# Kernel optimization log

Hardware: AMD Instinct MI355X
Metric: run time of the kernel (lower is better)

## Reference

```python
import jax, jax.numpy as jnp
import numpy as np

B = 65536
D = 512            # resnet18 fc.in_features
NUM_CLASSES = 512  # size of batch_centers
LEVELS = [2048, 1024, 512]


def setup_inputs() -> dict:
    key = jax.random.key(0)
    ks = jax.random.split(key, 8)
    x = jax.random.normal(ks[0], (B, D), dtype=jnp.float32)
    labels = jax.random.randint(ks[1], (B,), 0, NUM_CLASSES, dtype=jnp.int64)
    W0 = jax.random.normal(ks[2], (LEVELS[0], D), dtype=jnp.float32) * 0.02
    b0 = jnp.zeros((LEVELS[0],), dtype=jnp.float32)
    W1 = jax.random.normal(ks[3], (LEVELS[1], LEVELS[0]), dtype=jnp.float32) * 0.02
    b1 = jnp.zeros((LEVELS[1],), dtype=jnp.float32)
    W2 = jax.random.normal(ks[4], (LEVELS[2], LEVELS[1]), dtype=jnp.float32) * 0.02
    b2 = jnp.zeros((LEVELS[2],), dtype=jnp.float32)
    lambda_values = jnp.array([1e-3, 1.0, 1.0, 1.0], dtype=jnp.float32)
    return {"x": x, "W0": W0, "b0": b0, "W1": W1, "b1": b1,
            "W2": W2, "b2": b2, "lambda_values": lambda_values,
            "labels": labels}


def _cross_entropy(logits, labels):
    # mean over batch of -log p(label) (torch CrossEntropyLoss default)
    logp = jax.nn.log_softmax(logits, axis=-1)
    nll = -jnp.take_along_axis(logp, labels[:, None], axis=-1)[:, 0]
    return jnp.mean(nll)


def reference(x, W0, b0, W1, b1, W2, b2, lambda_values, labels):
    # --- per-class scatter-mean centers (vectorized segment reduce) ---
    sums = jax.ops.segment_sum(x, labels, num_segments=NUM_CLASSES)
    counts = jax.ops.segment_sum(jnp.ones((x.shape[0],), x.dtype), labels,
                                 num_segments=NUM_CLASSES)
    centers = jnp.where(counts[:, None] > 0,
                        sums / jnp.maximum(counts, 1.0)[:, None],
                        0.0)  # classes absent from batch keep zero centers
    # --- gather-diff center loss: sum_i ||x_i - c_{y_i}||^2 ---
    diff = x - centers[labels]
    center_loss = jnp.sum(diff * diff)
    # --- cascaded classification heads, CE at each level ---
    h = x
    losses = []
    for W, b in ((W0, b0), (W1, b1), (W2, b2)):
        h = h @ W.T + b
        losses.append(_cross_entropy(h, labels))
    classification_losses = jnp.stack(losses)
    return lambda_values[0] * center_loss + jnp.dot(lambda_values[1:],
                                                    classification_losses)
```

## Files before the change

### kernel.cpp

```cpp
#include <hip/hip_runtime.h>
#include <cstdint>
#include <cstddef>

using f32x4  = __attribute__((ext_vector_type(4))) float;
using i32x4v = __attribute__((ext_vector_type(4))) int;
using i32x8v = __attribute__((ext_vector_type(8))) int;

__device__ __forceinline__ unsigned char f2fp8(float f) {
  return (unsigned char)(__builtin_amdgcn_cvt_pk_fp8_f32(f, f, 0, false) & 0xff);
}

__device__ __forceinline__ float fp8b0(unsigned int w) {
  return __builtin_amdgcn_cvt_f32_fp8(w, 0);
}
__device__ __forceinline__ float fp8b1(unsigned int w) {
  return __builtin_amdgcn_cvt_f32_fp8(w, 1);
}
__device__ __forceinline__ float fp8b2(unsigned int w) {
  return __builtin_amdgcn_cvt_f32_fp8(w, 2);
}
__device__ __forceinline__ float fp8b3(unsigned int w) {
  return __builtin_amdgcn_cvt_f32_fp8(w, 3);
}

__device__ __forceinline__ float waveRed(float v) {
#pragma unroll
  for (int m = 32; m >= 1; m >>= 1) v += __shfl_xor(v, m, 64);
  return v;
}

__device__ __forceinline__ void gload16(const void* g, void* l) {
  __builtin_amdgcn_global_load_lds(
      (__attribute__((address_space(1))) uint32_t*)(uintptr_t)g,
      (__attribute__((address_space(3))) uint32_t*)(uint32_t*)l,
      16, 0, 0);
}

__global__ __launch_bounds__(256) void prep_w(
    const float4* __restrict__ W1, const float4* __restrict__ W2,
    const float4* __restrict__ W0f4, const float* __restrict__ W0,
    const float* __restrict__ b0,
    uint32_t* __restrict__ W1_8, uint32_t* __restrict__ W2_8,
    uint32_t* __restrict__ W0_8, unsigned char* __restrict__ W0t8,
    float* __restrict__ zr, int zwords, float* __restrict__ biascat) {
  __shared__ unsigned char t8[64][65];
  const int b = blockIdx.x;
  const int tid = threadIdx.x;
  if (b < 1024) {
    for (int i = b * 256 + tid; i < 524288; i += 1024 * 256) {
      float4 v = W1[i];
      int p = __builtin_amdgcn_cvt_pk_fp8_f32(v.x, v.y, 0, false);
      p = __builtin_amdgcn_cvt_pk_fp8_f32(v.z, v.w, p, true);
      W1_8[i] = (uint32_t)p;
    }
  } else if (b < 1280) {
    for (int i = (b - 1024) * 256 + tid; i < 131072; i += 256 * 256) {
      float4 v = W2[i];
      int p = __builtin_amdgcn_cvt_pk_fp8_f32(v.x, v.y, 0, false);
      p = __builtin_amdgcn_cvt_pk_fp8_f32(v.z, v.w, p, true);
      W2_8[i] = (uint32_t)p;
    }
  } else if (b < 1536) {
    for (int i = (b - 1280) * 256 + tid; i < 262144; i += 256 * 256) {
      float4 v = W0f4[i];
      int p = __builtin_amdgcn_cvt_pk_fp8_f32(v.x, v.y, 0, false);
      p = __builtin_amdgcn_cvt_pk_fp8_f32(v.z, v.w, p, true);
      W0_8[i] = (uint32_t)p;
    }
  } else if (b < 1792) {
    const int t = b - 1536;
    const int r0 = (t >> 3) * 64, c0 = (t & 7) * 64;
#pragma unroll
    for (int p = 0; p < 16; ++p) {
      const int row = p * 4 + (tid >> 6), col = tid & 63;
      t8[row][col] = f2fp8(W0[(size_t)(r0 + row) * 512 + c0 + col]);
    }
    __syncthreads();
#pragma unroll
    for (int p = 0; p < 16; ++p) {
      const int oc = p * 4 + (tid >> 6), orr = tid & 63;
      W0t8[(size_t)(c0 + oc) * 2048 + r0 + orr] = t8[orr][oc];
    }
  } else {
    const int zb = (zwords + 255) >> 8;
    if (b < 1792 + zb) {
      const int i = (b - 1792) * 256 + tid;
      if (i < zwords) zr[i] = 0.f;
    } else {
      const int i = (b - 1792 - zb) * 256 + tid;
      if (i < 2048) biascat[i] = b0[i];
    }
  }
}

__global__ __launch_bounds__(256) void count_k(const int* __restrict__ lab,
                                               int* __restrict__ counts, int n) {
  __shared__ int h[512];
  for (int i = threadIdx.x; i < 512; i += 256) h[i] = 0;
  __syncthreads();
  for (int i = blockIdx.x * 256 + threadIdx.x; i < n; i += gridDim.x * 256)
    atomicAdd(&h[lab[i]], 1);
  __syncthreads();
  for (int i = threadIdx.x; i < 512; i += 256) {
    int v = h[i];
    if (v) atomicAdd(&counts[i], v);
  }
}

__global__ void prefix_k(const int* __restrict__ counts, int* __restrict__ offsets,
                         int* __restrict__ cursor, int nc) {
  const int lane = threadIdx.x;
  int base = 0;
  for (int c0 = 0; c0 < nc; c0 += 64) {
    int v = counts[c0 + lane];
    int x = v;
#pragma unroll
    for (int d = 1; d < 64; d <<= 1) {
      int y = __shfl_up(x, d, 64);
      if (lane >= d) x += y;
    }
    int excl = base + x - v;
    offsets[c0 + lane] = excl;
    cursor[c0 + lane] = excl;
    base += __shfl(x, 63, 64);
  }
}

__global__ void scatter_k(const int* __restrict__ lab, int* __restrict__ cursor,
                          int* __restrict__ buckets, int n) {
  for (int i = blockIdx.x * 256 + threadIdx.x; i < n; i += gridDim.x * 256) {
    int pos = atomicAdd(&cursor[lab[i]], 1);
    buckets[pos] = i;
  }
}

__global__ __launch_bounds__(256) void csum_k(const float* __restrict__ x,
    const int* __restrict__ buckets, const int* __restrict__ offsets,
    const int* __restrict__ counts, float* __restrict__ centers,
    float* __restrict__ scal) {
  const int c = blockIdx.x >> 2, q = blockIdx.x & 3;
  const int cnt = counts[c];
  const int t = threadIdx.x;
  float sx = 0.f, sy = 0.f, ssq = 0.f;
  int lo = 0, hi = 0;
  if (cnt) {
    const int beg = offsets[c];
    lo = beg + (cnt * q) / 4;
    hi = beg + (cnt * (q + 1)) / 4;
    for (int i = lo; i < hi; ++i) {
      const int row = buckets[i];
      const float2 v = ((const float2*)(x + (size_t)row * 512))[t];
      sx += v.x;
      sy += v.y;
      ssq += v.x * v.x + v.y * v.y;
    }
    if (lo < hi) {
      atomicAdd(&centers[c * 512 + 2 * t], sx);
      atomicAdd(&centers[c * 512 + 2 * t + 1], sy);
    }
  }
  ssq = waveRed(ssq);
  __shared__ float red[4];
  if ((t & 63) == 0) red[t >> 6] = ssq;
  __syncthreads();
  if (t == 0) {
    const float s = red[0] + red[1] + red[2] + red[3];
    if (s != 0.f) atomicAdd(&scal[0], s);
  }
}

__global__ __launch_bounds__(256) void cnorm_k(const float* __restrict__ centers,
    const int* __restrict__ counts, float* __restrict__ out) {
  const int c = blockIdx.x;
  const int cnt = counts[c];
  if (cnt == 0) return;
  const float2 v = ((const float2*)(centers + (size_t)c * 512))[threadIdx.x];
  float ssq = v.x * v.x + v.y * v.y;
  ssq = waveRed(ssq);
  __shared__ float red[4];
  if ((threadIdx.x & 63) == 0) red[threadIdx.x >> 6] = ssq;
  __syncthreads();
  if (threadIdx.x == 0)
    atomicAdd(out, (red[0] + red[1] + red[2] + red[3]) / (float)cnt);
}

__global__ __launch_bounds__(256) void matvec_k(const float* __restrict__ W,
    const float* __restrict__ vin, const float* __restrict__ badd,
    float* __restrict__ vout, int K) {
  int row = blockIdx.x;
  float s = 0.f;
  for (int k = threadIdx.x; k < K; k += 256) s += W[(size_t)row * K + k] * vin[k];
  s = waveRed(s);
  __shared__ float red[4];
  if ((threadIdx.x & 63) == 0) red[threadIdx.x >> 6] = s;
  __syncthreads();
  if (threadIdx.x == 0) vout[row] = red[0] + red[1] + red[2] + red[3] + badd[row];
}

__global__ void pk_k(const float* __restrict__ centers,
                     const unsigned char* __restrict__ Bcat8,
                     const float* __restrict__ biascat,
                     const int* __restrict__ counts, float* __restrict__ scal) {
  const int b = blockIdx.x;
  const int lvl = b >> 9;
  const int c = b & 511;
  const int lane = threadIdx.x;
  const int cbase = (lvl == 0) ? 0 : (lvl == 1) ? 2048 : 3072;
  const float4* S = (const float4*)(centers + (size_t)c * 512);
  const uint2 wb = ((const uint2*)(Bcat8 + (size_t)(cbase + c) * 512))[lane];
  const float4 s0 = S[lane * 2];
  const float4 s1 = S[lane * 2 + 1];
  float s = s0.x * fp8b0(wb.x) + s0.y * fp8b1(wb.x) +
            s0.z * fp8b2(wb.x) + s0.w * fp8b3(wb.x) +
            s1.x * fp8b0(wb.y) + s1.y * fp8b1(wb.y) +
            s1.z * fp8b2(wb.y) + s1.w * fp8b3(wb.y);
  s = waveRed(s);
  if (lane == 0)
    atomicAdd(&scal[5 + lvl], s + (float)counts[c] * biascat[cbase + c]);
}

__global__ __launch_bounds__(256) void gemm8_w(
    const unsigned char* __restrict__ A8, const unsigned char* __restrict__ B8,
    int M, int N, int K, unsigned char* __restrict__ C8,
    unsigned char* __restrict__ Ct8) {
  __shared__ __align__(16) unsigned char As[128 * 128];
  __shared__ __align__(16) unsigned char Bs[128 * 128];
  const int tid = threadIdx.x;
  const int lane = tid & 63;
  const int wave = tid >> 6;
  const int lane16 = lane & 15;
  const int quad = lane >> 4;
  const int wm = (wave >> 1) * 64;
  const int wn = (wave & 1) * 64;
  const int m0 = blockIdx.y * 128;
  const int n0 = blockIdx.x * 128;

  f32x4 acc[4][4] = {};

  int srow[4], goff[4];
#pragma unroll
  for (int q = 0; q < 4; ++q) {
    const int s = tid + q * 256;
    const int row = s >> 3;
    const int c16 = s & 7;
    srow[q] = row;
    goff[q] = (((c16 >> 1) ^ (row & 3)) << 5) + ((c16 & 1) << 4);
  }

  for (int kt = 0; kt < K; kt += 128) {
#pragma unroll
    for (int q = 0; q < 4; ++q) {
      const int s = tid + q * 256;
      gload16(A8 + (size_t)(m0 + srow[q]) * K + kt + goff[q], &As[s * 16]);
      gload16(B8 + (size_t)(n0 + srow[q]) * K + kt + goff[q], &Bs[s * 16]);
    }
    __syncthreads();
    i32x8v a8[4], b8[4];
#pragma unroll
    for (int i = 0; i < 4; ++i) {
      const int row = i * 16 + lane16;
      const int sc = quad ^ (row & 3);
      const unsigned char* pa = &As[row * 128 + sc * 32];
      const i32x4v lo = *(const i32x4v*)pa;
      const i32x4v hi = *(const i32x4v*)(pa + 16);
      a8[i] = (i32x8v){lo[0], lo[1], lo[2], lo[3], hi[0], hi[1], hi[2], hi[3]};
    }
#pragma unroll
    for (int j = 0; j < 4; ++j) {
      const int row = j * 16 + lane16;
      const int sc = quad ^ (row & 3);
      const unsigned char* pb = &Bs[row * 128 + sc * 32];
      const i32x4v lo = *(const i32x4v*)pb;
      const i32x4v hi = *(const i32x4v*)(pb + 16);
      b8[j] = (i32x8v){lo[0], lo[1], lo[2], lo[3], hi[0], hi[1], hi[2], hi[3]};
    }
#pragma unroll
    for (int i = 0; i < 4; ++i)
#pragma unroll
      for (int j = 0; j < 4; ++j)
        acc[i][j] = __builtin_amdgcn_mfma_scale_f32_16x16x128_f8f6f4(
            a8[i], b8[j], acc[i][j], 0, 0, 0, 0x7f7f7f7f, 0, 0x7f7f7f7f);
    __syncthreads();
  }
#pragma unroll
  for (int i = 0; i < 4; ++i)
#pragma unroll
    for (int r = 0; r < 4; ++r) {
      const int rowg = m0 + wm + i * 16 + quad * 4 + r;
#pragma unroll
      for (int j = 0; j < 4; ++j) {
        const int colg = n0 + wn + j * 16 + lane16;
        const unsigned char v8 = f2fp8(acc[i][j][r]);
        C8[(size_t)rowg * N + colg] = v8;
        if (Ct8) Ct8[(size_t)colg * M + rowg] = v8;
      }
    }
}

__global__ void reorder_k(const unsigned char* __restrict__ in,
                          unsigned char* __restrict__ out) {
  const int id = blockIdx.x * 256 + threadIdx.x;
  const int col = id >> 4;
  const int k32 = id & 15;
  const int kt = k32 >> 2, quad = k32 & 3;
  const size_t src = (size_t)col * 512 + k32 * 32;
  const size_t dst = (size_t)(col >> 6) * 32768 + (size_t)kt * 8192 +
                     (size_t)((col >> 4) & 3) * 2048 +
                     (size_t)(quad * 16 + (col & 15)) * 32;
  const uint4 a = *(const uint4*)(in + src);
  const uint4 b = *(const uint4*)(in + src + 16);
  *(uint4*)(out + dst) = a;
  *(uint4*)(out + dst + 16) = b;
}

__global__ __launch_bounds__(256, 2) void gemm_ce8(
    const float* __restrict__ x, const unsigned char* __restrict__ Bp,
    const float* __restrict__ bias, float* __restrict__ scal) {
  const int tid = threadIdx.x;
  const int lane = tid & 63;
  const int wave = tid >> 6;
  const int lane16 = lane & 15;
  const int quad = lane >> 4;
  const int m0 = blockIdx.x * 128 + wave * 32;

  i32x8v a[2][4];
#pragma unroll
  for (int i = 0; i < 2; ++i) {
    const float* xr = x + (size_t)(m0 + i * 16 + lane16) * 512 + quad * 32;
#pragma unroll
    for (int kt = 0; kt < 4; ++kt) {
      const float4* p4 = (const float4*)(xr + kt * 128);
      int d[8];
#pragma unroll
      for (int p = 0; p < 8; ++p) {
        const float4 f = p4[p];
        int w_ = __builtin_amdgcn_cvt_pk_fp8_f32(f.x, f.y, 0, false);
        w_ = __builtin_amdgcn_cvt_pk_fp8_f32(f.z, f.w, w_, true);
        d[p] = w_;
      }
      a[i][kt] = (i32x8v){d[0], d[1], d[2], d[3], d[4], d[5], d[6], d[7]};
    }
  }

  const unsigned char* bp = Bp + lane * 32;
  i32x8v bc[4], bn[4];
#pragma unroll
  for (int j = 0; j < 4; ++j) bc[j] = *(const i32x8v*)(bp + j * 2048);
  bp += 8192;

  float es[8];
#pragma unroll
  for (int k = 0; k < 8; ++k) es[k] = 0.f;

  int tile = 0;
#pragma unroll 1
  for (int lvl = 0; lvl < 3; ++lvl) {
    const int nt = (lvl == 0) ? 32 : (lvl == 1) ? 16 : 8;
#pragma unroll 1
    for (int t = 0; t < nt; ++t, ++tile) {
      f32x4 acc[2][4] = {};
#pragma unroll
      for (int kt2 = 0; kt2 < 2; ++kt2) {
#pragma unroll
        for (int j = 0; j < 4; ++j) bn[j] = *(const i32x8v*)(bp + j * 2048);
        bp += 8192;
#pragma unroll
        for (int i = 0; i < 2; ++i)
#pragma unroll
          for (int j = 0; j < 4; ++j)
            acc[i][j] = __builtin_amdgcn_mfma_scale_f32_16x16x128_f8f6f4(
                a[i][kt2 * 2], bc[j], acc[i][j], 0, 0, 0, 0x7f7f7f7f, 0,
                0x7f7f7f7f);
#pragma unroll
        for (int j = 0; j < 4; ++j) bc[j] = *(const i32x8v*)(bp + j * 2048);
        bp += 8192;
#pragma unroll
        for (int i = 0; i < 2; ++i)
#pragma unroll
          for (int j = 0; j < 4; ++j)
            acc[i][j] = __builtin_amdgcn_mfma_scale_f32_16x16x128_f8f6f4(
                a[i][kt2 * 2 + 1], bn[j], acc[i][j], 0, 0, 0, 0x7f7f7f7f, 0,
                0x7f7f7f7f);
      }
      float bj[4];
#pragma unroll
      for (int j = 0; j < 4; ++j) bj[j] = bias[tile * 64 + j * 16 + lane16];
#pragma unroll
      for (int i = 0; i < 2; ++i)
#pragma unroll
        for (int r = 0; r < 4; ++r) {
          float e = 0.f;
#pragma unroll
          for (int j = 0; j < 4; ++j) e += __expf(acc[i][j][r] + bj[j]);
          es[i * 4 + r] += e;
        }
      __builtin_amdgcn_s_barrier();
    }
    float ls = 0.f;
#pragma unroll
    for (int k = 0; k < 8; ++k) {
      float tot = es[k];
      tot += __shfl_xor(tot, 1, 64);
      tot += __shfl_xor(tot, 2, 64);
      tot += __shfl_xor(tot, 4, 64);
      tot += __shfl_xor(tot, 8, 64);
      if (lane16 == 0) ls += __logf(tot);
      es[k] = 0.f;
    }
    ls = waveRed(ls);
    if (lane == 0) atomicAdd(&scal[2 + lvl], ls);
  }
}

__global__ void fin_k(const float* __restrict__ scal, const float* __restrict__ lam,
                      float* __restrict__ out, float invB) {
  if (threadIdx.x == 0 && blockIdx.x == 0)
    out[0] = lam[0] * (scal[0] - scal[1]) +
             (lam[1] * (scal[2] - scal[5]) + lam[2] * (scal[3] - scal[6]) +
              lam[3] * (scal[4] - scal[7])) * invB;
}

extern "C" void kernel_launch(void* const* d_in, const int* in_sizes, int n_in,
                              void* d_out, int out_size, void* d_ws, size_t ws_size,
                              hipStream_t stream) {
  const float* x   = (const float*)d_in[0];
  const float* W0  = (const float*)d_in[1];
  const float* b0  = (const float*)d_in[2];
  const float* W1  = (const float*)d_in[3];
  const float* b1  = (const float*)d_in[4];
  const float* W2  = (const float*)d_in[5];
  const float* b2  = (const float*)d_in[6];
  const float* lam = (const float*)d_in[7];
  const int*   lab = (const int*)d_in[8];

  const int Bsz = in_sizes[8];
  const int D   = in_sizes[0] / Bsz;
  const int N0  = in_sizes[2];
  const int N1  = in_sizes[4];
  const int N2  = in_sizes[6];
  const int Ncat = N0 + N1 + N2;
  const int NCLS = 512;

  char* w = (char*)d_ws;
  size_t off = 0;
  auto alloc = [&](size_t bytes) -> void* {
    void* p = w + off;
    off += (bytes + 255) & ~(size_t)255;
    return p;
  };

  unsigned char* Bcat8 = (unsigned char*)alloc((size_t)Ncat * D);
  unsigned char* Bp    = (unsigned char*)alloc((size_t)Ncat * D + 16384);
  unsigned char* W1_8  = (unsigned char*)alloc((size_t)N1 * N0);
  unsigned char* W2_8  = (unsigned char*)alloc((size_t)N2 * N1);
  unsigned char* W0t8  = (unsigned char*)alloc((size_t)D * N0);
  unsigned char* M1t8  = (unsigned char*)alloc((size_t)D * N1);
  float* biascat = (float*)alloc((size_t)Ncat * 4);
  int* offsets = (int*)alloc(NCLS * 4);
  int* cursor  = (int*)alloc(NCLS * 4);
  int* buckets = (int*)alloc((size_t)Bsz * 4);
  const int zwords = NCLS + 8 + NCLS * 512;
  char* zr = (char*)alloc((size_t)zwords * 4);
  int*   counts  = (int*)zr;
  float* scal    = (float*)(zr + NCLS * 4);
  float* centers = (float*)(zr + NCLS * 4 + 32);
  (void)ws_size; (void)n_in; (void)out_size;

  const int zb = (zwords + 255) / 256;
  prep_w<<<dim3(1792 + zb + 8), dim3(256), 0, stream>>>(
      (const float4*)W1, (const float4*)W2, (const float4*)W0, W0, b0,
      (uint32_t*)W1_8, (uint32_t*)W2_8, (uint32_t*)Bcat8, W0t8,
      (float*)zr, zwords, biascat);

  count_k<<<dim3(32), dim3(256), 0, stream>>>(lab, counts, Bsz);
  prefix_k<<<dim3(1), dim3(64), 0, stream>>>(counts, offsets, cursor, NCLS);
  scatter_k<<<dim3(256), dim3(256), 0, stream>>>(lab, cursor, buckets, Bsz);
  csum_k<<<dim3(4 * NCLS), dim3(256), 0, stream>>>(x, buckets, offsets, counts,
                                                   centers, scal);
  cnorm_k<<<dim3(NCLS), dim3(256), 0, stream>>>(centers, counts, &scal[1]);

  matvec_k<<<dim3(N1), dim3(256), 0, stream>>>(W1, b0, b1, biascat + N0, N0);
  matvec_k<<<dim3(N2), dim3(256), 0, stream>>>(W2, biascat + N0, b2, biascat + N0 + N1, N1);

  gemm8_w<<<dim3(D / 128, N1 / 128), dim3(256), 0, stream>>>(
      W1_8, W0t8, N1, D, N0, Bcat8 + (size_t)N0 * D, M1t8);
  gemm8_w<<<dim3(D / 128, N2 / 128), dim3(256), 0, stream>>>(
      W2_8, M1t8, N2, D, N1, Bcat8 + (size_t)(N0 + N1) * D, nullptr);

  reorder_k<<<dim3(Ncat * D / 32 / 256), dim3(256), 0, stream>>>(Bcat8, Bp);

  pk_k<<<dim3(3 * NCLS), dim3(64), 0, stream>>>(centers, Bcat8, biascat,
                                                counts, scal);

  gemm_ce8<<<dim3(Bsz / 128), dim3(256), 0, stream>>>(x, Bp, biascat, scal);

  fin_k<<<dim3(1), dim3(64), 0, stream>>>(scal, lam, (float*)d_out, 1.f / (float)Bsz);
}
```

Baseline: 539.7 us.

## Stage B fragments through LDS with async prefetch; replace center atomics with partials

The fused GEMM+CE kernel now streams the packed fp8 weight fragments into a four-slot shared-memory ring using async global-to-LDS loads, waiting with vmcnt and barriers, instead of each wave loading its B fragments directly from global into registers. The bias vector is cached in shared memory once per block. The reorder kernel changes the packed layout to split each lane's 32 bytes into two 16-byte halves to match the 16-byte async loads. Separately, the per-class center sums write four partial buffers that cnorm_k reduces, replacing float atomics. The ring adds LDS traffic and a barrier per k-step, and may lower occupancy.

```diff
diff --git a/kernel.cpp b/kernel.cpp
--- a/kernel.cpp
+++ b/kernel.cpp
@@ -136,17 +136,15 @@
 
 __global__ __launch_bounds__(256) void csum_k(const float* __restrict__ x,
     const int* __restrict__ buckets, const int* __restrict__ offsets,
-    const int* __restrict__ counts, float* __restrict__ centers,
+    const int* __restrict__ counts, float* __restrict__ centers4,
     float* __restrict__ scal) {
   const int c = blockIdx.x >> 2, q = blockIdx.x & 3;
   const int cnt = counts[c];
   const int t = threadIdx.x;
   float sx = 0.f, sy = 0.f, ssq = 0.f;
-  int lo = 0, hi = 0;
   if (cnt) {
     const int beg = offsets[c];
-    lo = beg + (cnt * q) / 4;
-    hi = beg + (cnt * (q + 1)) / 4;
+    const int lo = beg + (cnt * q) / 4, hi = beg + (cnt * (q + 1)) / 4;
     for (int i = lo; i < hi; ++i) {
       const int row = buckets[i];
       const float2 v = ((const float2*)(x + (size_t)row * 512))[t];
@@ -154,11 +152,9 @@
       sy += v.y;
       ssq += v.x * v.x + v.y * v.y;
     }
-    if (lo < hi) {
-      atomicAdd(&centers[c * 512 + 2 * t], sx);
-      atomicAdd(&centers[c * 512 + 2 * t + 1], sy);
-    }
-  }
+  }
+  float2* dst = (float2*)(centers4 + (size_t)((c << 2) + q) * 512);
+  dst[t] = make_float2(sx, sy);
   ssq = waveRed(ssq);
   __shared__ float red[4];
   if ((t & 63) == 0) red[t >> 6] = ssq;
@@ -169,18 +165,25 @@
   }
 }
 
-__global__ __launch_bounds__(256) void cnorm_k(const float* __restrict__ centers,
-    const int* __restrict__ counts, float* __restrict__ out) {
+__global__ __launch_bounds__(256) void cnorm_k(const float* __restrict__ centers4,
+    float* __restrict__ centers, const int* __restrict__ counts,
+    float* __restrict__ out) {
   const int c = blockIdx.x;
+  const int t = threadIdx.x;
+  const float2* p = (const float2*)(centers4 + (size_t)(c << 2) * 512);
+  float2 s = p[t];
+  float2 s1 = p[t + 256], s2 = p[t + 512], s3 = p[t + 768];
+  s.x += s1.x + s2.x + s3.x;
+  s.y += s1.y + s2.y + s3.y;
+  ((float2*)(centers + (size_t)c * 512))[t] = s;
   const int cnt = counts[c];
   if (cnt == 0) return;
-  const float2 v = ((const float2*)(centers + (size_t)c * 512))[threadIdx.x];
-  float ssq = v.x * v.x + v.y * v.y;
+  float ssq = s.x * s.x + s.y * s.y;
   ssq = waveRed(ssq);
   __shared__ float red[4];
-  if ((threadIdx.x & 63) == 0) red[threadIdx.x >> 6] = ssq;
+  if ((t & 63) == 0) red[t >> 6] = ssq;
   __syncthreads();
-  if (threadIdx.x == 0)
+  if (t == 0)
     atomicAdd(out, (red[0] + red[1] + red[2] + red[3]) / (float)cnt);
 }
 
@@ -303,25 +306,29 @@
   const int col = id >> 4;
   const int k32 = id & 15;
   const int kt = k32 >> 2, quad = k32 & 3;
+  const int l = quad * 16 + (col & 15);
   const size_t src = (size_t)col * 512 + k32 * 32;
-  const size_t dst = (size_t)(col >> 6) * 32768 + (size_t)kt * 8192 +
-                     (size_t)((col >> 4) & 3) * 2048 +
-                     (size_t)(quad * 16 + (col & 15)) * 32;
+  const size_t fragbase = (size_t)(col >> 6) * 32768 + (size_t)kt * 8192 +
+                          (size_t)((col >> 4) & 3) * 2048;
   const uint4 a = *(const uint4*)(in + src);
   const uint4 b = *(const uint4*)(in + src + 16);
-  *(uint4*)(out + dst) = a;
-  *(uint4*)(out + dst + 16) = b;
+  *(uint4*)(out + fragbase + l * 16) = a;
+  *(uint4*)(out + fragbase + 1024 + l * 16) = b;
 }
 
 __global__ __launch_bounds__(256, 2) void gemm_ce8(
     const float* __restrict__ x, const unsigned char* __restrict__ Bp,
     const float* __restrict__ bias, float* __restrict__ scal) {
+  __shared__ __align__(16) unsigned char Bl[4][8192];
+  __shared__ float biasl[3584];
   const int tid = threadIdx.x;
   const int lane = tid & 63;
   const int wave = tid >> 6;
   const int lane16 = lane & 15;
   const int quad = lane >> 4;
   const int m0 = blockIdx.x * 128 + wave * 32;
+
+  for (int i = tid; i < 3584; i += 256) biasl[i] = bias[i];
 
   i32x8v a[2][4];
 #pragma unroll
@@ -341,12 +348,12 @@
       a[i][kt] = (i32x8v){d[0], d[1], d[2], d[3], d[4], d[5], d[6], d[7]};
     }
   }
-
-  const unsigned char* bp = Bp + lane * 32;
-  i32x8v bc[4], bn[4];
-#pragma unroll
-  for (int j = 0; j < 4; ++j) bc[j] = *(const i32x8v*)(bp + j * 2048);
-  bp += 8192;
+  __syncthreads();
+
+  const int soff = wave * 2048 + lane * 16;
+  gload16(Bp + soff, &Bl[0][soff]);
+  gload16(Bp + soff + 1024, &Bl[0][soff + 1024]);
+  const unsigned char* bsrc = Bp + soff + 8192;
 
   float es[8];
 #pragma unroll
@@ -360,31 +367,33 @@
     for (int t = 0; t < nt; ++t, ++tile) {
       f32x4 acc[2][4] = {};
 #pragma unroll
-      for (int kt2 = 0; kt2 < 2; ++kt2) {
-#pragma unroll
-        for (int j = 0; j < 4; ++j) bn[j] = *(const i32x8v*)(bp + j * 2048);
-        bp += 8192;
+      for (int ks = 0; ks < 4; ++ks) {
+        const int nslot = (ks + 1) & 3;
+        gload16(bsrc, &Bl[nslot][soff]);
+        gload16(bsrc + 1024, &Bl[nslot][soff + 1024]);
+        bsrc += 8192;
+        asm volatile("s_waitcnt vmcnt(2)" ::: "memory");
+        asm volatile("s_barrier" ::: "memory");
+        const unsigned char* bb = &Bl[ks][0];
+        i32x8v b8[4];
+#pragma unroll
+        for (int j = 0; j < 4; ++j) {
+          const i32x4v lo = *(const i32x4v*)(bb + j * 2048 + lane * 16);
+          const i32x4v hi = *(const i32x4v*)(bb + j * 2048 + 1024 + lane * 16);
+          b8[j] = (i32x8v){lo[0], lo[1], lo[2], lo[3],
+                           hi[0], hi[1], hi[2], hi[3]};
+        }
 #pragma unroll
         for (int i = 0; i < 2; ++i)
 #pragma unroll
           for (int j = 0; j < 4; ++j)
             acc[i][j] = __builtin_amdgcn_mfma_scale_f32_16x16x128_f8f6f4(
-                a[i][kt2 * 2], bc[j], acc[i][j], 0, 0, 0, 0x7f7f7f7f, 0,
-                0x7f7f7f7f);
-#pragma unroll
-        for (int j = 0; j < 4; ++j) bc[j] = *(const i32x8v*)(bp + j * 2048);
-        bp += 8192;
-#pragma unroll
-        for (int i = 0; i < 2; ++i)
-#pragma unroll
-          for (int j = 0; j < 4; ++j)
-            acc[i][j] = __builtin_amdgcn_mfma_scale_f32_16x16x128_f8f6f4(
-                a[i][kt2 * 2 + 1], bn[j], acc[i][j], 0, 0, 0, 0x7f7f7f7f, 0,
+                a[i][ks], b8[j], acc[i][j], 0, 0, 0, 0x7f7f7f7f, 0,
                 0x7f7f7f7f);
       }
       float bj[4];
 #pragma unroll
-      for (int j = 0; j < 4; ++j) bj[j] = bias[tile * 64 + j * 16 + lane16];
+      for (int j = 0; j < 4; ++j) bj[j] = biasl[tile * 64 + j * 16 + lane16];
 #pragma unroll
       for (int i = 0; i < 2; ++i)
 #pragma unroll
@@ -394,7 +403,6 @@
           for (int j = 0; j < 4; ++j) e += __expf(acc[i][j][r] + bj[j]);
           es[i * 4 + r] += e;
         }
-      __builtin_amdgcn_s_barrier();
     }
     float ls = 0.f;
 #pragma unroll
@@ -455,15 +463,16 @@
   unsigned char* W2_8  = (unsigned char*)alloc((size_t)N2 * N1);
   unsigned char* W0t8  = (unsigned char*)alloc((size_t)D * N0);
   unsigned char* M1t8  = (unsigned char*)alloc((size_t)D * N1);
-  float* biascat = (float*)alloc((size_t)Ncat * 4);
+  float* biascat  = (float*)alloc((size_t)Ncat * 4);
   int* offsets = (int*)alloc(NCLS * 4);
   int* cursor  = (int*)alloc(NCLS * 4);
   int* buckets = (int*)alloc((size_t)Bsz * 4);
-  const int zwords = NCLS + 8 + NCLS * 512;
+  float* centers4 = (float*)alloc((size_t)NCLS * 512 * 4 * 4);
+  float* centers  = (float*)alloc((size_t)NCLS * 512 * 4);
+  const int zwords = NCLS + 8;
   char* zr = (char*)alloc((size_t)zwords * 4);
   int*   counts  = (int*)zr;
   float* scal    = (float*)(zr + NCLS * 4);
-  float* centers = (float*)(zr + NCLS * 4 + 32);
   (void)ws_size; (void)n_in; (void)out_size;
 
   const int zb = (zwords + 255) / 256;
@@ -476,8 +485,9 @@
   prefix_k<<<dim3(1), dim3(64), 0, stream>>>(counts, offsets, cursor, NCLS);
   scatter_k<<<dim3(256), dim3(256), 0, stream>>>(lab, cursor, buckets, Bsz);
   csum_k<<<dim3(4 * NCLS), dim3(256), 0, stream>>>(x, buckets, offsets, counts,
-                                                   centers, scal);
-  cnorm_k<<<dim3(NCLS), dim3(256), 0, stream>>>(centers, counts, &scal[1]);
+                                                   centers4, scal);
+  cnorm_k<<<dim3(NCLS), dim3(256), 0, stream>>>(centers4, centers, counts,
+                                                &scal[1]);
 
   matvec_k<<<dim3(N1), dim3(256), 0, stream>>>(W1, b0, b1, biascat + N0, N0);
   matvec_k<<<dim3(N2), dim3(256), 0, stream>>>(W2, biascat + N0, b2, biascat + N0 + N1, N1);
```

Measured after the change: 517.2 us. -4.2%, faster.
